# Kernel optimization log

Measured on AMD Instinct MI355X. Metric: run time of the kernel, lower is better.

## Reference

```python
import jax, jax.numpy as jnp
import numpy as np

P = 16        # patch size
IMG = 224     # image H=W
C = 3         # channels
D = 768       # projection_dim (= patch flatten dim here)
H = 12        # num heads
M = D // 4    # new_size = flattened_size / shrink_ratio(4) = 192
L = 6         # transformer layers
N = (IMG // P) ** 2   # 196 patches
FF = 3072     # dense_units[0]
HEAD = 512    # dense_units[2]
NCLS = 1000
EPS = 1e-6
B = 32


def setup_inputs() -> dict:
    key = jax.random.key(0)
    ks = iter(jax.random.split(key, 40))
    u = lambda shape, s=0.02: jax.random.uniform(next(ks), shape, jnp.float32, -s, s)
    image = jax.random.normal(next(ks), (B, IMG, IMG, C), jnp.float32)
    return dict(
        image=image,
        patch_w=u((P * P * C, D)), patch_b=u((D,)), pos_emb=u((N, D)),
        qw=u((L, D, M, H)), qb=jnp.zeros((L, M, H), jnp.float32),
        kw=u((L, D, M, H)), kb=jnp.zeros((L, M, H), jnp.float32),
        vw=u((L, D, M, H)), vb=jnp.zeros((L, M, H), jnp.float32),
        ow1=u((L, H * N, N)), ob1=jnp.zeros((L, M, N), jnp.float32),
        ow2=u((L, M, D)), ob2=jnp.zeros((L, N, D), jnp.float32),
        d1w=u((L, D, FF)), d1b=u((L, FF)),
        d2w=u((L, FF, D)), d2b=u((L, D)),
        head_w=u((N * D, HEAD), 0.005), head_b=u((HEAD,)),
        cls_w=u((HEAD, NCLS)), cls_b=u((NCLS,)),
    )


def _ln(x):
    # ViT_Custom_LayerNormalization: moments over axes [0,1,2] (all elements of [B,N,D])
    m = jnp.mean(x)
    v = jnp.mean(jnp.square(x - m))
    return (x - m) / jnp.sqrt(v + EPS)


def _gelu(x):
    return jax.nn.gelu(x, approximate=False)  # keras 'gelu' default is exact


def _forward(image, patch_w, patch_b, pos_emb, qw, qb, kw, kb, vw, vb,
             ow1, ob1, ow2, ob2, d1w, d1b, d2w, d2b, head_w, head_b, cls_w, cls_b):
    b = image.shape[0]
    # tf.image.extract_patches with VALID, stride=patch: [B,N,p*p*C] row-major patches
    patches = image.reshape(b, IMG // P, P, IMG // P, P, C)
    patches = patches.transpose(0, 1, 3, 2, 4, 5).reshape(b, N, P * P * C)
    x = patches @ patch_w + patch_b + pos_emb  # patch encode + pos embedding
    scale = 1.0 / np.float32(np.sqrt(D))       # key_dim = projection_dim
    for l in range(L):
        x1 = _ln(x)
        # per-head 3-D tensordot projections: [B,N,D] x [D,M,H] -> [B,N,M,H]
        q = jnp.einsum('bnd,dmh->bnmh', x1, qw[l]) + qb[l]
        k = jnp.einsum('bnd,dmh->bnmh', x1, kw[l]) + kb[l]
        v = jnp.einsum('bnd,dmh->bnmh', x1, vw[l]) + vb[l]
        att = jnp.einsum('bnmh,bNmh->bhnN', q, k) * scale  # [B,H,N,N]
        a = jax.nn.softmax(att, axis=-1)
        # attn @ V, then the module's transpose/unstack-concat -> [B,M,H*N] head-major
        o = jnp.einsum('bhnN,bNmh->bmhn', a, v).reshape(b, M, H * N)
        t = (o @ ow1[l] + ob1[l]).transpose(0, 2, 1)  # [B,N,M]
        attn_out = t @ ow2[l] + ob2[l]                # [B,N,D]
        x2 = attn_out + x
        x3 = _ln(x2)
        h = _gelu(x3 @ d1w[l] + d1b[l])
        h = _gelu(h @ d2w[l] + d2b[l])
        x = h + x2
    x = _ln(x)
    flat = x.reshape(b, N * D)
    feat = _gelu(flat @ head_w + head_b)
    return feat @ cls_w + cls_b  # [B, NCLS]


def reference(image, patch_w, patch_b, pos_emb, qw, qb, kw, kb, vw, vb,
              ow1, ob1, ow2, ob2, d1w, d1b, d2w, d2b, head_w, head_b, cls_w, cls_b):
    return _forward(image, patch_w, patch_b, pos_emb, qw, qb, kw, kb, vw, vb,
                    ow1, ob1, ow2, ob2, d1w, d1b, d2w, d2b, head_w, head_b, cls_w, cls_b)
```

## Files before the change

kernel.cpp:

```cpp
#include <hip/hip_runtime.h>
#include <cmath>

#define BZ    32
#define NP    196
#define DDIM  768
#define NHEAD 12
#define MDIM  192
#define NLAY  6
#define FFDIM 3072
#define HEADU 512
#define NCLS  1000
#define KHEAD 150528
#define BND   4816896
#define NPART 294

typedef __bf16 bf16_t;
typedef __bf16 bf16x8 __attribute__((ext_vector_type(8)));
typedef __bf16 bf16x4 __attribute__((ext_vector_type(4)));
typedef float  f32x4  __attribute__((ext_vector_type(4)));
typedef float  f32x2  __attribute__((ext_vector_type(2)));

#define OB_X      0L
#define OB_R      19267584L
#define OB_XB     38535168L
#define OB_XQKV   48168960L
#define OB_VT     134873088L
#define OB_O      165543936L
#define OB_T      194641920L
#define OB_WQKV   197050368L
#define OB_WO1    260751360L
#define OB_WO2    268025856L
#define OB_WD1    269795328L
#define OB_WD2    298106880L
#define OB_WPAT   326418432L
#define OB_BQKV   327598080L
#define OB_OB1T   327763968L
#define OB_RED    328667136L
#define OB_FEAT   328675584L

#define VT_SSTRIDE  39936L
#define ATTN_LDSP   93184
#define ATTN_LDS    143360
#define G256_LDS    98304
#define XROW        13824

__device__ __forceinline__ float gelu_exact(float x){
    return 0.5f * x * (1.0f + erff(x * 0.70710678118654752f));
}

__device__ __forceinline__ void gld16(const void* g, void* l){
    __builtin_amdgcn_global_load_lds((const __attribute__((address_space(1))) void*)g,
                                     (__attribute__((address_space(3))) void*)l, 16, 0, 0);
}

__global__ void __launch_bounds__(256)
patch_extract_k(const float* __restrict__ img, bf16_t* __restrict__ out)
{
    long idx = (long)blockIdx.x * 256 + threadIdx.x;
    if (idx >= (long)BND) return;
    int k = (int)(idx % DDIM);
    long bn = idx / DDIM;
    int n = (int)(bn % NP);
    int b = (int)(bn / NP);
    int c  = k % 3;
    int pj = (k / 3) % 16;
    int pi = k / 48;
    int gi = n / 14, gj = n % 14;
    long src = (((long)(b * 224 + gi * 16 + pi)) * 224 + (gj * 16 + pj)) * 3 + c;
    out[idx] = (bf16_t)img[src];
}

__global__ void __launch_bounds__(256)
wconv_k(const float* __restrict__ in, bf16_t* __restrict__ out,
        int IR, int IC, long OLD, int perm, int padTo, long inZ, long outZ)
{
    __shared__ float tile[32][33];
    int tid = threadIdx.x, tx = tid & 31, ty = tid >> 5;
    int c0 = blockIdx.x * 32, r0 = blockIdx.y * 32;
    const float* inz = in + (long)blockIdx.z * inZ;
    bf16_t* outz = out + (long)blockIdx.z * outZ;
    #pragma unroll
    for (int i = 0; i < 4; i++){
        int r = r0 + ty + 8*i, c = c0 + tx;
        tile[ty + 8*i][tx] = (r < IR && c < IC) ? inz[(long)r * IC + c] : 0.f;
    }
    __syncthreads();
    #pragma unroll
    for (int i = 0; i < 4; i++){
        int c = c0 + ty + 8*i, r = r0 + tx;
        if (c < IC && r < padTo){
            long pc = perm ? (long)(c % 12) * 192 + c / 12 : (long)c;
            outz[pc * OLD + r] = (bf16_t)tile[tx][ty + 8*i];
        }
    }
}

__global__ void __launch_bounds__(256)
gather_bias_k(const float* __restrict__ qb, const float* __restrict__ kb,
              const float* __restrict__ vb, float* __restrict__ out)
{
    int tid = blockIdx.x * 256 + threadIdx.x;
    int l = blockIdx.y;
    if (tid >= 6912) return;
    int g = tid / 2304, w = tid % 2304;
    int h = w / 192, m = w % 192;
    const float* src = (g == 0) ? qb : (g == 1) ? kb : vb;
    out[l*6912 + tid] = src[l*2304 + m * 12 + h];
}

__global__ void __launch_bounds__(256)
tr_bias_k(const float* __restrict__ ob1, float* __restrict__ out)
{
    int idx = blockIdx.x * 256 + threadIdx.x;
    int l = blockIdx.y;
    if (idx >= 37632) return;
    int n = idx / 192, m = idx - n*192;
    out[(long)l*37632 + idx] = ob1[(long)l*37632 + m*196 + n];
}

__global__ void __launch_bounds__(256)
zero_pad_o_k(bf16_t* __restrict__ o)
{
    int idx = blockIdx.x * 256 + threadIdx.x;
    if (idx >= 6144*16) return;
    int r = idx >> 4, j = idx & 15;
    o[(long)r * 2368 + 2352 + j] = (bf16_t)0.f;
}

__global__ void __launch_bounds__(256)
tr_v_k(const bf16_t* __restrict__ X, bf16_t* __restrict__ VT)
{
    __shared__ bf16_t tile[32][33];
    int tid = threadIdx.x, tx = tid & 31, ty = tid >> 5;
    int s = blockIdx.z, b = s & 31, h = s >> 5;
    int m0 = blockIdx.x * 32, n0 = blockIdx.y * 32;
    #pragma unroll
    for (int i = 0; i < 4; i++){
        int r = n0 + ty + 8*i, c = m0 + tx;
        tile[ty + 8*i][tx] = (r < 196) ?
            X[(long)(b*196 + r) * 6912 + 4608 + h*192 + c] : (bf16_t)0.f;
    }
    __syncthreads();
    #pragma unroll
    for (int i = 0; i < 4; i++){
        int m = m0 + ty + 8*i, n = n0 + tx;
        if (n < 208)
            VT[(long)s * VT_SSTRIDE + (long)m * 208 + n] = tile[tx][ty + 8*i];
    }
}

__global__ void __launch_bounds__(256)
ln_apply_k(const float* __restrict__ x, bf16_t* __restrict__ yb, float* __restrict__ yf,
           const float* __restrict__ psum, const float* __restrict__ psq, int npart)
{
    __shared__ float sred[8];
    int tid = threadIdx.x;
    float s = 0.f, q = 0.f;
    for (int i = tid; i < npart; i += 256){ s += psum[i]; q += psq[i]; }
    #pragma unroll
    for (int off = 32; off > 0; off >>= 1){ s += __shfl_xor(s, off); q += __shfl_xor(q, off); }
    if ((tid & 63) == 0){ sred[(tid>>6)*2] = s; sred[(tid>>6)*2+1] = q; }
    __syncthreads();
    s = sred[0] + sred[2] + sred[4] + sred[6];
    q = sred[1] + sred[3] + sred[5] + sred[7];
    float mean = s / (float)BND;
    float inv  = rsqrtf(q / (float)BND - mean*mean + 1e-6f);

    long i = (long)blockIdx.x * 256 + tid;
    if (i >= BND / 4) return;
    float4 v = ((const float4*)x)[i];
    v.x = (v.x - mean) * inv;
    v.y = (v.y - mean) * inv;
    v.z = (v.z - mean) * inv;
    v.w = (v.w - mean) * inv;
    bf16x4 o4 = { (bf16_t)v.x, (bf16_t)v.y, (bf16_t)v.z, (bf16_t)v.w };
    ((bf16x4*)yb)[i] = o4;
    if (yf) ((float4*)yf)[i] = v;
}

__global__ void __launch_bounds__(256)
attn_fused_k(const bf16_t* __restrict__ XQKV, const bf16_t* __restrict__ VT,
             bf16_t* __restrict__ O)
{
    extern __shared__ char lds[];
    const int tid = threadIdx.x, lane = tid & 63, w = tid >> 6;
    const int fr = lane & 15, kc = lane >> 4;
    const int s = blockIdx.y, qhalf = blockIdx.x;
    const int q0 = qhalf * 112;
    const int b = s & 31, h = s >> 5;
    const float scale = 0.03608439182435161f;
    const char* Xb = (const char*)XQKV + (long)(b*196) * XROW;
    const char* Qs = Xb + h*384;
    const char* Ks = Xb + 4608 + h*384;
    const char* Vs = (const char*)(VT + (long)s * VT_SSTRIDE);

    for (int t = 0; t < 23; t++){
        int idx = t*256 + tid;
        if (idx < 5824){
            int row = idx / 28, sl = idx - row*28;
            bool val = (sl < 24) && (row < 196);
            const char* src = Ks + (val ? ((long)row*XROW + ((sl*16) ^ ((row & 7) << 4))) : 0);
            gld16(src, lds + idx*16);
        }
    }
    asm volatile("s_waitcnt vmcnt(0)");
    __syncthreads();

    float pv_all[2][13][4];
    #pragma unroll
    for (int ii = 0; ii < 2; ii++){
        int i = w + ii*4;
        if (i >= 7) continue;
        f32x4 sa[13];
        #pragma unroll
        for (int f = 0; f < 13; f++) sa[f] = (f32x4){0.f,0.f,0.f,0.f};
        int qr = q0 + i*16 + fr; if (qr > 195) qr = 195;
        #pragma unroll
        for (int c = 0; c < 6; c++){
            bf16x8 av = *(const bf16x8*)(Qs + (long)qr*XROW + c*64 + kc*16);
            #pragma unroll
            for (int f = 0; f < 13; f++){
                int krow = f*16 + fr;
                bf16x8 bv = *(const bf16x8*)(lds + krow*448 + ((c*64 + kc*16) ^ ((krow & 7) << 4)));
                sa[f] = __builtin_amdgcn_mfma_f32_16x16x32_bf16(av, bv, sa[f], 0, 0, 0);
            }
        }
        #pragma unroll
        for (int r = 0; r < 4; r++){
            float mx = -1e30f;
            #pragma unroll
            for (int f = 0; f < 13; f++)
                if (f*16 + fr < 196) mx = fmaxf(mx, sa[f][r] * scale);
            mx = fmaxf(mx, __shfl_xor(mx, 1));
            mx = fmaxf(mx, __shfl_xor(mx, 2));
            mx = fmaxf(mx, __shfl_xor(mx, 4));
            mx = fmaxf(mx, __shfl_xor(mx, 8));
            float sum = 0.f;
            #pragma unroll
            for (int f = 0; f < 13; f++){
                float pv = (f*16 + fr < 196) ? __expf(sa[f][r] * scale - mx) : 0.f;
                pv_all[ii][f][r] = pv; sum += pv;
            }
            sum += __shfl_xor(sum, 1);
            sum += __shfl_xor(sum, 2);
            sum += __shfl_xor(sum, 4);
            sum += __shfl_xor(sum, 8);
            float inv = 1.f / sum;
            #pragma unroll
            for (int f = 0; f < 13; f++) pv_all[ii][f][r] *= inv;
        }
        #pragma unroll
        for (int f = 0; f < 13; f++)
            #pragma unroll
            for (int r = 0; r < 4; r++){
                int row = i*16 + kc*4 + r;
                int cb = (f*16 + fr) * 2;
                int a = ATTN_LDSP + row*448 + (cb < 384 ? (cb ^ ((row & 7) << 4)) : cb);
                *(bf16_t*)(lds + a) = (bf16_t)pv_all[ii][f][r];
            }
        if (lane < 32){
            int row = i*16 + (lane >> 1);
            *(f32x4*)(lds + ATTN_LDSP + row*448 + 416 + (lane & 1)*16) = (f32x4){0.f,0.f,0.f,0.f};
        }
    }
    __syncthreads();

    for (int t = 0; t < 21; t++){
        int idx = t*256 + tid;
        int row = idx / 28, sl = idx - row*28;
        bool val = (sl < 26);
        int cb = (sl < 24) ? ((sl*16) ^ ((row & 7) << 4)) : sl*16;
        const char* src = Vs + (val ? (row*416 + cb) : 0);
        gld16(src, lds + idx*16);
    }
    asm volatile("s_waitcnt vmcnt(0)");
    __syncthreads();

    f32x4 oa2[2][12];
    #pragma unroll
    for (int ii = 0; ii < 2; ii++){
        int i = w + ii*4;
        #pragma unroll
        for (int f = 0; f < 12; f++) oa2[ii][f] = (f32x4){0.f,0.f,0.f,0.f};
        if (i >= 7) continue;
        #pragma unroll
        for (int c = 0; c < 7; c++){
            int prow = i*16 + fr;
            int cb = c*64 + kc*16;
            int acb = (cb < 384) ? (cb ^ ((prow & 7) << 4)) : cb;
            bf16x8 av = *(const bf16x8*)(lds + ATTN_LDSP + prow*448 + acb);
            #pragma unroll
            for (int f = 0; f < 12; f++){
                int vrow = f*16 + fr;
                int bcb = (cb < 384) ? (cb ^ ((vrow & 7) << 4)) : cb;
                bf16x8 bv = *(const bf16x8*)(lds + vrow*448 + bcb);
                oa2[ii][f] = __builtin_amdgcn_mfma_f32_16x16x32_bf16(av, bv, oa2[ii][f], 0, 0, 0);
            }
        }
    }
    __syncthreads();

    #pragma unroll
    for (int ii = 0; ii < 2; ii++){
        int i = w + ii*4;
        if (i >= 7) continue;
        #pragma unroll
        for (int f = 0; f < 12; f++){
            int m = f*16 + fr;
            #pragma unroll
            for (int r = 0; r < 4; r++){
                int nl = i*16 + kc*4 + r;
                *(bf16_t*)(lds + m*232 + nl*2) = (bf16_t)oa2[ii][f][r];
            }
        }
    }
    __syncthreads();
    const int nch = (qhalf == 0) ? 28 : 21;
    const int total = 192 * nch;
    char* ob = (char*)O + ((long)(b*192))*4736 + ((long)(h*196 + q0))*2;
    for (int idx = tid; idx < total; idx += 256){
        int m = idx / nch, ch = idx - m*nch;
        f32x2 v2 = *(const f32x2*)(lds + m*232 + ch*8);
        *(f32x2*)(ob + (long)m*4736 + ch*8) = v2;
    }
}

__global__ void __launch_bounds__(512, 2)
gemm256_k(const bf16_t* __restrict__ A, long ldA,
          const bf16_t* __restrict__ B, long ldB,
          bf16_t* __restrict__ C, long ldC,
          const float* __restrict__ bias1,
          int Md, int Nd, int Kd, int G, int doGelu)
{
    extern __shared__ char gsm[];
    const int tid = threadIdx.x;
    const int lane = tid & 63, w = tid >> 6;
    const int wm = w >> 2, wn = w & 3;

    int gx = gridDim.x, gy = gridDim.y;
    int n2d = gx * gy;
    int flat = blockIdx.x + gx * blockIdx.y;
    int q8 = n2d >> 3, r8 = n2d & 7;
    int xcd = flat & 7, pos = flat >> 3;
    int lid = (xcd < r8 ? xcd*(q8+1) : r8*(q8+1) + (xcd-r8)*q8) + pos;
    int fullg = gx / G;
    int fullsz = fullg * G * gy;
    int bx, by;
    if (lid < fullsz){
        int gsz = G * gy;
        int g = lid / gsz, rem = lid - g*gsz;
        by = rem / G; bx = g*G + (rem - by*G);
    } else {
        int tw = gx - fullg*G;
        int rem = lid - fullsz;
        by = rem / tw; bx = fullg*G + (rem - by*tw);
    }
    const int row0 = by * 256, col0 = bx * 256;

    f32x4 acc[8][4];
    #pragma unroll
    for (int i = 0; i < 8; i++)
        #pragma unroll
        for (int j = 0; j < 4; j++)
            acc[i][j] = (f32x4){0.f, 0.f, 0.f, 0.f};

    const int fr = lane & 15, kc = lane >> 4;
    const int swz = (fr >> 1) & 3;
    int aOff[8], bOff[4];
    #pragma unroll
    for (int i = 0; i < 8; i++)
        aOff[i] = (wm*128 + i*16 + fr) * 64 + ((kc ^ swz) << 4);
    #pragma unroll
    for (int j = 0; j < 4; j++)
        bOff[j] = (wn*64 + j*16 + fr) * 64 + ((kc ^ swz) << 4);

    auto stage = [&](int buf, int kt){
        long kOff = (long)kt * 32;
        char* base = gsm + buf * 32768;
        #pragma unroll
        for (int r = 0; r < 2; r++){
            int idx = r*512 + tid;
            int row = idx >> 2, cp = idx & 3;
            int cc = cp ^ ((row >> 1) & 3);
            int ar = row0 + row; if (ar >= Md) ar = Md - 1;
            int br = col0 + row; if (br >= Nd) br = Nd - 1;
            gld16((const void*)(A + (long)ar*ldA + kOff + cc*8), (void*)(base + row*64 + cp*16));
            gld16((const void*)(B + (long)br*ldB + kOff + cc*8), (void*)(base + 16384 + row*64 + cp*16));
        }
    };

    const int nt = Kd >> 5;
    stage(0, 0);
    stage(1, 1);
    asm volatile("s_waitcnt vmcnt(4)" ::: "memory");
    __builtin_amdgcn_s_barrier();
    __builtin_amdgcn_sched_barrier(0);

    for (int t = 0; t < nt; t++){
        int cur = t % 3;
        if (t + 2 < nt) stage((t + 2) % 3, t + 2);
        const char* baseA = gsm + cur * 32768;
        const char* baseB = baseA + 16384;
        bf16x8 av[8], bv[4];
        #pragma unroll
        for (int i = 0; i < 8; i++) av[i] = *(const bf16x8*)(baseA + aOff[i]);
        #pragma unroll
        for (int j = 0; j < 4; j++) bv[j] = *(const bf16x8*)(baseB + bOff[j]);
        __builtin_amdgcn_s_setprio(1);
        #pragma unroll
        for (int i = 0; i < 8; i++)
            #pragma unroll
            for (int j = 0; j < 4; j++)
                acc[i][j] = __builtin_amdgcn_mfma_f32_16x16x32_bf16(av[i], bv[j], acc[i][j], 0, 0, 0);
        __builtin_amdgcn_s_setprio(0);
        if (t + 2 < nt)      asm volatile("s_waitcnt vmcnt(4)" ::: "memory");
        else if (t + 1 < nt) asm volatile("s_waitcnt vmcnt(0)" ::: "memory");
        __builtin_amdgcn_s_barrier();
        __builtin_amdgcn_sched_barrier(0);
    }

    #pragma unroll
    for (int i = 0; i < 8; i++){
        int gmb = row0 + wm*128 + i*16 + kc*4;
        #pragma unroll
        for (int j = 0; j < 4; j++){
            int gn = col0 + wn*64 + j*16 + fr;
            if (gn >= Nd) continue;
            float b1 = bias1 ? bias1[gn] : 0.f;
            #pragma unroll
            for (int r = 0; r < 4; r++){
                int gm = gmb + r;
                if (gm >= Md) continue;
                float v = acc[i][j][r] + b1;
                if (doGelu) v = gelu_exact(v);
                C[(long)gm*ldC + gn] = (bf16_t)v;
            }
        }
    }
}

__global__ void __launch_bounds__(256)
mfma_gemm_k(const bf16_t* __restrict__ A, long ldA, long sA,
            const bf16_t* __restrict__ B, long ldB, long sB,
            void* __restrict__ C, long ldC, long sC,
            const float* __restrict__ Cadd,
            const float* __restrict__ bias1,
            const float* __restrict__ bias2, int b2mod, int b2ld,
            int Md, int Nd, int Kd, float alpha, int doGelu, int mode,
            float* __restrict__ psum, float* __restrict__ psq, int redN, int G)
{
    __shared__ bf16_t sm[3][2][128][32];
    __shared__ float redbuf[8];
    const int tid = threadIdx.x;
    const int lane = tid & 63, w = tid >> 6;
    const int wm = w >> 1, wn = w & 1;
    const int z = blockIdx.z;

    int n2d = gridDim.x * gridDim.y;
    int flat = blockIdx.x + gridDim.x * blockIdx.y;
    int q8 = n2d >> 3, r8 = n2d & 7;
    int xcd = flat & 7, pos = flat >> 3;
    int lid = (xcd < r8 ? xcd*(q8+1) : r8*(q8+1) + (xcd-r8)*q8) + pos;
    int gx = gridDim.x, gy = gridDim.y;
    int fullg = gx / G;
    int fullsz = fullg * G * gy;
    int bx, by;
    if (lid < fullsz){
        int gsz = G * gy;
        int g = lid / gsz, rem = lid - g*gsz;
        by = rem / G; bx = g*G + (rem - by*G);
    } else {
        int tw = gx - fullg*G;
        int rem = lid - fullsz;
        by = rem / tw; bx = fullg*G + (rem - by*tw);
    }

    const int row0 = by * 128, col0 = bx * 128;

    const bf16_t* Ab = A + (long)z * sA + (long)row0 * ldA;
    const bf16_t* Bb = B + (long)z * sB + (long)col0 * ldB;

    f32x4 acc[4][4];
    #pragma unroll
    for (int i = 0; i < 4; i++)
        #pragma unroll
        for (int j = 0; j < 4; j++)
            acc[i][j] = (f32x4){0.f, 0.f, 0.f, 0.f};

    const int fr = lane & 15, kc = lane >> 4;
    const int swz = (fr >> 1) & 3;
    int aOff[4], bOff[4];
    #pragma unroll
    for (int i = 0; i < 4; i++){
        aOff[i] = (wm*64 + i*16 + fr) * 64 + ((kc ^ swz) << 4);
        bOff[i] = (wn*64 + i*16 + fr) * 64 + ((kc ^ swz) << 4);
    }

    auto stage = [&](int buf, int kt){
        long kOff = (long)kt * 32;
        #pragma unroll
        for (int r = 0; r < 2; r++){
            int idx = r*256 + tid;
            int row = idx >> 2, cp = idx & 3;
            int cc = cp ^ ((row >> 1) & 3);
            gld16((const void*)(Ab + (long)row*ldA + kOff + cc*8), (void*)&sm[buf][0][row][cp*8]);
            gld16((const void*)(Bb + (long)row*ldB + kOff + cc*8), (void*)&sm[buf][1][row][cp*8]);
        }
    };

    const int nt = Kd >> 5;
    stage(0, 0);
    stage(1, 1);
    asm volatile("s_waitcnt vmcnt(4)" ::: "memory");
    __builtin_amdgcn_s_barrier();
    __builtin_amdgcn_sched_barrier(0);

    for (int t = 0; t < nt; t++){
        int cur = t % 3;
        if (t + 2 < nt) stage((t + 2) % 3, t + 2);
        const char* baseA = (const char*)sm + cur * 16384;
        const char* baseB = baseA + 8192;
        bf16x8 av[4], bv[4];
        #pragma unroll
        for (int i = 0; i < 4; i++){
            av[i] = *(const bf16x8*)(baseA + aOff[i]);
            bv[i] = *(const bf16x8*)(baseB + bOff[i]);
        }
        __builtin_amdgcn_s_setprio(1);
        #pragma unroll
        for (int i = 0; i < 4; i++)
            #pragma unroll
            for (int j = 0; j < 4; j++)
                acc[i][j] = __builtin_amdgcn_mfma_f32_16x16x32_bf16(av[i], bv[j], acc[i][j], 0, 0, 0);
        __builtin_amdgcn_s_setprio(0);
        if (t + 2 < nt)      asm volatile("s_waitcnt vmcnt(4)" ::: "memory");
        else if (t + 1 < nt) asm volatile("s_waitcnt vmcnt(0)" ::: "memory");
        __builtin_amdgcn_s_barrier();
        __builtin_amdgcn_sched_barrier(0);
    }

    float rs = 0.f, rq = 0.f;
    #pragma unroll
    for (int i = 0; i < 4; i++){
        int gmb = row0 + wm*64 + i*16 + kc*4;
        #pragma unroll
        for (int j = 0; j < 4; j++){
            int gn = col0 + wn*64 + j*16 + fr;
            if (gn >= Nd) continue;
            #pragma unroll
            for (int r = 0; r < 4; r++){
                int gm = gmb + r;
                if (gm >= Md) continue;
                float v = alpha * acc[i][j][r];
                if (bias1) v += bias1[gn];
                if (bias2) v += bias2[(long)(gm % b2mod) * b2ld + gn];
                if (doGelu) v = gelu_exact(v);
                if (mode == 0){
                    long off = (long)z*sC + (long)gm*ldC + gn;
                    if (Cadd) v += Cadd[off];
                    ((float*)C)[off] = v;
                    rs += v; rq += v*v;
                } else {
                    ((bf16_t*)C)[(long)z*sC + (long)gm*ldC + gn] = (bf16_t)v;
                }
            }
        }
    }

    if (redN > 0){
        #pragma unroll
        for (int off = 32; off > 0; off >>= 1){
            rs += __shfl_xor(rs, off); rq += __shfl_xor(rq, off);
        }
        if (lane == 0){ redbuf[w] = rs; redbuf[4 + w] = rq; }
        __syncthreads();
        if (tid == 0){
            psum[flat] = redbuf[0] + redbuf[1] + redbuf[2] + redbuf[3];
            psq[flat]  = redbuf[4] + redbuf[5] + redbuf[6] + redbuf[7];
        }
    }
}

__global__ void __launch_bounds__(256)
gemm64_k(const bf16_t* __restrict__ A, long ldA, long sA,
         const bf16_t* __restrict__ B, long ldB, long sB,
         bf16_t* __restrict__ C, long ldC, long sC,
         const float* __restrict__ bias2, int b2ld,
         int Md, int Nd, int Kd)
{
    __shared__ bf16_t sm[3][2][64][32];
    const int tid = threadIdx.x;
    const int lane = tid & 63, w = tid >> 6;
    const int wm = w >> 1, wn = w & 1;
    const int z = blockIdx.z;
    const int row0 = blockIdx.y * 64, col0 = blockIdx.x * 64;

    const bf16_t* Ab = A + (long)z * sA + (long)row0 * ldA;
    const bf16_t* Bb = B + (long)z * sB + (long)col0 * ldB;

    f32x4 acc[2][2];
    #pragma unroll
    for (int i = 0; i < 2; i++)
        #pragma unroll
        for (int j = 0; j < 2; j++)
            acc[i][j] = (f32x4){0.f,0.f,0.f,0.f};

    const int fr = lane & 15, kc = lane >> 4;
    const int swz = (fr >> 1) & 3;
    int aOff[2], bOff[2];
    #pragma unroll
    for (int i = 0; i < 2; i++){
        aOff[i] = (wm*32 + i*16 + fr) * 64 + ((kc ^ swz) << 4);
        bOff[i] = (wn*32 + i*16 + fr) * 64 + ((kc ^ swz) << 4);
    }

    auto stage = [&](int buf, int kt){
        long kOff = (long)kt * 32;
        int row = tid >> 2, cp = tid & 3;
        int cc = cp ^ ((row >> 1) & 3);
        gld16((const void*)(Ab + (long)row*ldA + kOff + cc*8), (void*)&sm[buf][0][row][cp*8]);
        gld16((const void*)(Bb + (long)row*ldB + kOff + cc*8), (void*)&sm[buf][1][row][cp*8]);
    };

    const int nt = Kd >> 5;
    stage(0, 0);
    stage(1, 1);
    asm volatile("s_waitcnt vmcnt(2)" ::: "memory");
    __builtin_amdgcn_s_barrier();
    __builtin_amdgcn_sched_barrier(0);

    for (int t = 0; t < nt; t++){
        int cur = t % 3;
        if (t + 2 < nt) stage((t + 2) % 3, t + 2);
        const char* baseA = (const char*)sm + cur * 8192;
        const char* baseB = baseA + 4096;
        bf16x8 av[2], bv[2];
        #pragma unroll
        for (int i = 0; i < 2; i++){
            av[i] = *(const bf16x8*)(baseA + aOff[i]);
            bv[i] = *(const bf16x8*)(baseB + bOff[i]);
        }
        __builtin_amdgcn_s_setprio(1);
        #pragma unroll
        for (int i = 0; i < 2; i++)
            #pragma unroll
            for (int j = 0; j < 2; j++)
                acc[i][j] = __builtin_amdgcn_mfma_f32_16x16x32_bf16(av[i], bv[j], acc[i][j], 0, 0, 0);
        __builtin_amdgcn_s_setprio(0);
        if (t + 2 < nt)      asm volatile("s_waitcnt vmcnt(2)" ::: "memory");
        else if (t + 1 < nt) asm volatile("s_waitcnt vmcnt(0)" ::: "memory");
        __builtin_amdgcn_s_barrier();
        __builtin_amdgcn_sched_barrier(0);
    }

    #pragma unroll
    for (int i = 0; i < 2; i++){
        int gmb = row0 + wm*32 + i*16 + kc*4;
        #pragma unroll
        for (int j = 0; j < 2; j++){
            int gn = col0 + wn*32 + j*16 + fr;
            if (gn >= Nd) continue;
            #pragma unroll
            for (int r = 0; r < 4; r++){
                int gm = gmb + r;
                if (gm >= Md) continue;
                float v = acc[i][j][r];
                if (bias2) v += bias2[(long)gm * b2ld + gn];
                C[(long)z*sC + (long)gm*ldC + gn] = (bf16_t)v;
            }
        }
    }
}

__global__ void __launch_bounds__(256)
head_splitk_k(const float* __restrict__ A, const float* __restrict__ W, float* __restrict__ feat)
{
    __shared__ float As[16][36];
    __shared__ float Bs[16][68];
    int col0 = blockIdx.x * 64;
    long kbase = (long)blockIdx.y * 2352;
    int tid = threadIdx.x, tx = tid & 15, ty = tid >> 4;
    float acc[2][4] = {};
    for (int k0 = 0; k0 < 2352; k0 += 16){
        #pragma unroll
        for (int u = 0; u < 2; u++){
            int idx = tid * 2 + u;
            int m = idx >> 4, kk = idx & 15;
            As[kk][m] = A[(long)m * KHEAD + kbase + k0 + kk];
        }
        #pragma unroll
        for (int u = 0; u < 4; u++){
            int idx = tid * 4 + u;
            int kk = idx >> 6, n = idx & 63;
            Bs[kk][n] = W[(kbase + k0 + kk) * 512 + col0 + n];
        }
        __syncthreads();
        #pragma unroll
        for (int kk = 0; kk < 16; kk++){
            float a0 = As[kk][ty*2], a1 = As[kk][ty*2+1];
            float b0 = Bs[kk][tx*4], b1 = Bs[kk][tx*4+1], b2 = Bs[kk][tx*4+2], b3 = Bs[kk][tx*4+3];
            acc[0][0] += a0*b0; acc[0][1] += a0*b1; acc[0][2] += a0*b2; acc[0][3] += a0*b3;
            acc[1][0] += a1*b0; acc[1][1] += a1*b1; acc[1][2] += a1*b2; acc[1][3] += a1*b3;
        }
        __syncthreads();
    }
    #pragma unroll
    for (int i = 0; i < 2; i++)
        #pragma unroll
        for (int j = 0; j < 4; j++)
            atomicAdd(&feat[(ty*2 + i) * 512 + col0 + tx*4 + j], acc[i][j]);
}

__global__ void __launch_bounds__(256)
cls_k(const float* __restrict__ feat, const float* __restrict__ hb,
      const float* __restrict__ W, const float* __restrict__ bias, float* __restrict__ out)
{
    __shared__ float fs[512];
    int b = blockIdx.y;
    int j = blockIdx.x * 256 + threadIdx.x;
    for (int i = threadIdx.x; i < 512; i += 256)
        fs[i] = gelu_exact(feat[b * 512 + i] + hb[i]);
    __syncthreads();
    if (j < NCLS){
        float s = bias[j];
        for (int k = 0; k < 512; k++) s += fs[k] * W[(long)k * NCLS + j];
        out[b * NCLS + j] = s;
    }
}

extern "C" void kernel_launch(void* const* d_in, const int* in_sizes, int n_in,
                              void* d_out, int out_size, void* d_ws, size_t ws_size,
                              hipStream_t stream)
{
    const float* image   = (const float*)d_in[0];
    const float* patch_w = (const float*)d_in[1];
    const float* patch_b = (const float*)d_in[2];
    const float* pos_emb = (const float*)d_in[3];
    const float* qw  = (const float*)d_in[4];
    const float* qb  = (const float*)d_in[5];
    const float* kw  = (const float*)d_in[6];
    const float* kb  = (const float*)d_in[7];
    const float* vw  = (const float*)d_in[8];
    const float* vb  = (const float*)d_in[9];
    const float* ow1 = (const float*)d_in[10];
    const float* ob1 = (const float*)d_in[11];
    const float* ow2 = (const float*)d_in[12];
    const float* ob2 = (const float*)d_in[13];
    const float* d1w = (const float*)d_in[14];
    const float* d1b = (const float*)d_in[15];
    const float* d2w = (const float*)d_in[16];
    const float* d2b = (const float*)d_in[17];
    const float* head_w = (const float*)d_in[18];
    const float* head_b = (const float*)d_in[19];
    const float* cls_w  = (const float*)d_in[20];
    const float* cls_b  = (const float*)d_in[21];

    char* wsb = (char*)d_ws;
    float*  X    = (float*) (wsb + OB_X);
    float*  R    = (float*) (wsb + OB_R);
    bf16_t* XB   = (bf16_t*)(wsb + OB_XB);
    bf16_t* XQKV = (bf16_t*)(wsb + OB_XQKV);
    bf16_t* VT   = (bf16_t*)(wsb + OB_VT);
    bf16_t* O    = (bf16_t*)(wsb + OB_O);
    bf16_t* Tt   = (bf16_t*)(wsb + OB_T);
    bf16_t* H1   = XQKV;
    bf16_t* PATB = XQKV;
    bf16_t* WQKV = (bf16_t*)(wsb + OB_WQKV);
    bf16_t* WO1  = (bf16_t*)(wsb + OB_WO1);
    bf16_t* WO2  = (bf16_t*)(wsb + OB_WO2);
    bf16_t* WD1  = (bf16_t*)(wsb + OB_WD1);
    bf16_t* WD2  = (bf16_t*)(wsb + OB_WD2);
    bf16_t* WPAT = (bf16_t*)(wsb + OB_WPAT);
    float*  BQKV = (float*) (wsb + OB_BQKV);
    float*  OB1T = (float*) (wsb + OB_OB1T);
    float*  PS   = (float*) (wsb + OB_RED);
    float*  PQ   = PS + 512;
    float*  FEAT = (float*) (wsb + OB_FEAT);
    float*  out  = (float*)d_out;

    hipFuncSetAttribute((const void*)attn_fused_k,
                        hipFuncAttributeMaxDynamicSharedMemorySize, ATTN_LDS);
    hipFuncSetAttribute((const void*)gemm256_k,
                        hipFuncAttributeMaxDynamicSharedMemorySize, G256_LDS);

    auto pickG = [](int Kd){
        int g = (3*1024*1024) / (128 * Kd * 2);
        if (g > 8) g = 8;
        if (g < 1) g = 1;
        return g;
    };
    auto mg = [&](const bf16_t* A, long ldA, long sA, const bf16_t* B, long ldB, long sB,
                  void* C, long ldC, long sC, const float* Cadd, const float* b1,
                  const float* b2, int b2mod, int b2ld,
                  int Md, int Nd, int Kd, int nb, float alpha, int gelu, int mode, int redN){
        dim3 g((Nd + 127) / 128, (Md + 127) / 128, nb);
        mfma_gemm_k<<<g, 256, 0, stream>>>(A, ldA, sA, B, ldB, sB, C, ldC, sC,
                                           Cadd, b1, b2, b2mod, b2ld,
                                           Md, Nd, Kd, alpha, gelu, mode, PS, PQ, redN,
                                           pickG(Kd));
    };
    auto wconv = [&](const float* in, bf16_t* o_, int IR, int IC, int perm, long OLD,
                     int padTo, int nz, long inZ, long outZ){
        dim3 g((IC + 31) / 32, (padTo + 31) / 32, nz);
        wconv_k<<<g, 256, 0, stream>>>(in, o_, IR, IC, OLD, perm, padTo, inZ, outZ);
    };
    auto lnapply = [&](const float* in, bf16_t* ob, float* of){
        ln_apply_k<<<4704, 256, 0, stream>>>(in, ob, of, PS, PQ, NPART);
    };

    wconv(patch_w, WPAT, 768, 768, 0, 768, 768, 1, 0, 0);
    wconv(qw, WQKV,               768, 2304, 1, 768, 768, 6, 768L*2304, 6912L*768);
    wconv(kw, WQKV + 2304L*768,   768, 2304, 1, 768, 768, 6, 768L*2304, 6912L*768);
    wconv(vw, WQKV + 4608L*768,   768, 2304, 1, 768, 768, 6, 768L*2304, 6912L*768);
    wconv(ow1, WO1, 2352, 196, 0, 2368, 2368, 6, 2352L*196, 606208L);
    wconv(ow2, WO2, 192, 768, 0, 192, 192, 6, 147456L, 147456L);
    wconv(d1w, WD1, 768, 3072, 0, 768, 768, 6, 2359296L, 2359296L);
    wconv(d2w, WD2, 3072, 768, 0, 3072, 3072, 6, 2359296L, 2359296L);
    gather_bias_k<<<dim3(27, 6), 256, 0, stream>>>(qb, kb, vb, BQKV);
    tr_bias_k<<<dim3(147, 6), 256, 0, stream>>>(ob1, OB1T);

    patch_extract_k<<<18816, 256, 0, stream>>>(image, PATB);
    mg(PATB, 768, 0, WPAT, 768, 0, X, 768, 0,
       nullptr, patch_b, pos_emb, 196, 768, 6272, 768, 768, 1, 1.f, 0, 0, NPART);
    zero_pad_o_k<<<384, 256, 0, stream>>>(O);

    for (int l = 0; l < NLAY; l++){
        lnapply(X, XB, nullptr);
        gemm256_k<<<dim3(27, 25), 512, G256_LDS, stream>>>(
            XB, 768, WQKV + (long)l*6912*768, 768, XQKV, 6912,
            BQKV + l*6912, 6272, 6912, 768, 4, 0);
        tr_v_k<<<dim3(6, 7, 384), 256, 0, stream>>>(XQKV, VT);
        attn_fused_k<<<dim3(2, 384), 256, ATTN_LDS, stream>>>(XQKV, VT, O);
        gemm64_k<<<dim3(3, 4, 32), 256, 0, stream>>>(
            WO1 + (long)l*606208, 2368, 0, O, 2368, 192L*2368, Tt, 192, 37632,
            OB1T + (long)l*37632, 192, 196, 192, 2368);
        mg(Tt, 192, 0, WO2 + (long)l*147456, 192, 0, R, 768, 0, X, nullptr,
           ob2 + (long)l*196*768, 196, 768, 6272, 768, 192, 1, 1.f, 0, 0, NPART);
        lnapply(R, XB, nullptr);
        gemm256_k<<<dim3(12, 25), 512, G256_LDS, stream>>>(
            XB, 768, WD1 + (long)l*2359296, 768, H1, 3072,
            d1b + l*3072, 6272, 3072, 768, 4, 1);
        mg(H1, 3072, 0, WD2 + (long)l*2359296, 3072, 0, X, 768, 0, R,
           d2b + l*768, nullptr, 1, 1, 6272, 768, 3072, 1, 1.f, 1, 0, NPART);
    }

    lnapply(X, XB, R);
    hipMemsetAsync(FEAT, 0, BZ * HEADU * sizeof(float), stream);
    head_splitk_k<<<dim3(8, 64), 256, 0, stream>>>(R, head_w, FEAT);
    cls_k<<<dim3(4, 32), 256, 0, stream>>>(FEAT, head_b, cls_w, cls_b, out);
    (void)in_sizes; (void)n_in; (void)out_size; (void)ws_size;
}
```

Measured before the change: 3.444 ms.

## Split-K the FFN down-projection and fuse bias, GELU, residual and LN stats

The second FFN GEMM (K=3072, only 6x49 tiles) now runs as a 2-way split-K, each half writing fp32 partials to a new workspace slice. A new elementwise kernel sums the partials, adds bias, applies GELU and the residual, and produces per-block LayerNorm partial sums, so ln_apply reads 4704 partials instead of 294. The first FFN GEMM moves from gemm256_k to the 128-tile mfma_gemm_k, and the QKV GEMM's grouping parameter goes from 4 to 8. The aim is more parallelism on the under-filled GEMM, at the cost of extra fp32 partial traffic and one more launch per layer.

```diff
diff --git a/kernel.cpp b/kernel.cpp
--- a/kernel.cpp
+++ b/kernel.cpp
@@ -13,6 +13,7 @@
 #define KHEAD 150528
 #define BND   4816896
 #define NPART 294
+#define NPARTF 4704
 
 typedef __bf16 bf16_t;
 typedef __bf16 bf16x8 __attribute__((ext_vector_type(8)));
@@ -24,6 +25,7 @@
 #define OB_R      19267584L
 #define OB_XB     38535168L
 #define OB_XQKV   48168960L
+#define OB_P0     86704128L
 #define OB_VT     134873088L
 #define OB_O      165543936L
 #define OB_T      194641920L
@@ -36,7 +38,7 @@
 #define OB_BQKV   327598080L
 #define OB_OB1T   327763968L
 #define OB_RED    328667136L
-#define OB_FEAT   328675584L
+#define OB_FEAT   328704768L
 
 #define VT_SSTRIDE  39936L
 #define ATTN_LDSP   93184
@@ -176,6 +178,36 @@
     bf16x4 o4 = { (bf16_t)v.x, (bf16_t)v.y, (bf16_t)v.z, (bf16_t)v.w };
     ((bf16x4*)yb)[i] = o4;
     if (yf) ((float4*)yf)[i] = v;
+}
+
+__global__ void __launch_bounds__(256)
+ffn2_finish_k(const float* __restrict__ P, const float* __restrict__ R,
+              const float* __restrict__ d2b, float* __restrict__ X,
+              float* __restrict__ psum, float* __restrict__ psq)
+{
+    __shared__ float redbuf[8];
+    int tid = threadIdx.x;
+    long i = (long)blockIdx.x * 256 + tid;
+    float4 a = ((const float4*)P)[i];
+    float4 b = ((const float4*)(P + 4816896))[i];
+    float4 r = ((const float4*)R)[i];
+    int col = (int)((i * 4) % 768);
+    float v0 = gelu_exact(a.x + b.x + d2b[col])     + r.x;
+    float v1 = gelu_exact(a.y + b.y + d2b[col + 1]) + r.y;
+    float v2 = gelu_exact(a.z + b.z + d2b[col + 2]) + r.z;
+    float v3 = gelu_exact(a.w + b.w + d2b[col + 3]) + r.w;
+    float4 o; o.x = v0; o.y = v1; o.z = v2; o.w = v3;
+    ((float4*)X)[i] = o;
+    float rs = v0 + v1 + v2 + v3;
+    float rq = v0*v0 + v1*v1 + v2*v2 + v3*v3;
+    #pragma unroll
+    for (int off = 32; off > 0; off >>= 1){ rs += __shfl_xor(rs, off); rq += __shfl_xor(rq, off); }
+    if ((tid & 63) == 0){ redbuf[(tid>>6)*2] = rs; redbuf[(tid>>6)*2+1] = rq; }
+    __syncthreads();
+    if (tid == 0){
+        psum[blockIdx.x] = redbuf[0] + redbuf[2] + redbuf[4] + redbuf[6];
+        psq[blockIdx.x]  = redbuf[1] + redbuf[3] + redbuf[5] + redbuf[7];
+    }
 }
 
 __global__ void __launch_bounds__(256)
@@ -456,6 +488,9 @@
     const int wm = w >> 1, wn = w & 1;
     const int z = blockIdx.z;
 
+    long kStart = 0; int KdL = Kd; long zA = z;
+    if (mode == 7){ kStart = (long)z * (Kd >> 1); KdL = Kd >> 1; zA = 0; }
+
     int n2d = gridDim.x * gridDim.y;
     int flat = blockIdx.x + gridDim.x * blockIdx.y;
     int q8 = n2d >> 3, r8 = n2d & 7;
@@ -477,8 +512,8 @@
 
     const int row0 = by * 128, col0 = bx * 128;
 
-    const bf16_t* Ab = A + (long)z * sA + (long)row0 * ldA;
-    const bf16_t* Bb = B + (long)z * sB + (long)col0 * ldB;
+    const bf16_t* Ab = A + zA * sA + (long)row0 * ldA + kStart;
+    const bf16_t* Bb = B + zA * sB + (long)col0 * ldB + kStart;
 
     f32x4 acc[4][4];
     #pragma unroll
@@ -508,7 +543,7 @@
         }
     };
 
-    const int nt = Kd >> 5;
+    const int nt = KdL >> 5;
     stage(0, 0);
     stage(1, 1);
     asm volatile("s_waitcnt vmcnt(4)" ::: "memory");
@@ -560,6 +595,8 @@
                     if (Cadd) v += Cadd[off];
                     ((float*)C)[off] = v;
                     rs += v; rq += v*v;
+                } else if (mode == 7){
+                    ((float*)C)[(long)z*sC + (long)gm*ldC + gn] = v;
                 } else {
                     ((bf16_t*)C)[(long)z*sC + (long)gm*ldC + gn] = (bf16_t)v;
                 }
@@ -760,6 +797,7 @@
     float*  R    = (float*) (wsb + OB_R);
     bf16_t* XB   = (bf16_t*)(wsb + OB_XB);
     bf16_t* XQKV = (bf16_t*)(wsb + OB_XQKV);
+    float*  P0   = (float*) (wsb + OB_P0);
     bf16_t* VT   = (bf16_t*)(wsb + OB_VT);
     bf16_t* O    = (bf16_t*)(wsb + OB_O);
     bf16_t* Tt   = (bf16_t*)(wsb + OB_T);
@@ -774,7 +812,7 @@
     float*  BQKV = (float*) (wsb + OB_BQKV);
     float*  OB1T = (float*) (wsb + OB_OB1T);
     float*  PS   = (float*) (wsb + OB_RED);
-    float*  PQ   = PS + 512;
+    float*  PQ   = PS + NPARTF;
     float*  FEAT = (float*) (wsb + OB_FEAT);
     float*  out  = (float*)d_out;
 
@@ -804,8 +842,8 @@
         dim3 g((IC + 31) / 32, (padTo + 31) / 32, nz);
         wconv_k<<<g, 256, 0, stream>>>(in, o_, IR, IC, OLD, perm, padTo, inZ, outZ);
     };
-    auto lnapply = [&](const float* in, bf16_t* ob, float* of){
-        ln_apply_k<<<4704, 256, 0, stream>>>(in, ob, of, PS, PQ, NPART);
+    auto lnapply = [&](const float* in, bf16_t* ob, float* of, int npart){
+        ln_apply_k<<<4704, 256, 0, stream>>>(in, ob, of, PS, PQ, npart);
     };
 
     wconv(patch_w, WPAT, 768, 768, 0, 768, 768, 1, 0, 0);
@@ -825,10 +863,10 @@
     zero_pad_o_k<<<384, 256, 0, stream>>>(O);
 
     for (int l = 0; l < NLAY; l++){
-        lnapply(X, XB, nullptr);
+        lnapply(X, XB, nullptr, l == 0 ? NPART : NPARTF);
         gemm256_k<<<dim3(27, 25), 512, G256_LDS, stream>>>(
             XB, 768, WQKV + (long)l*6912*768, 768, XQKV, 6912,
-            BQKV + l*6912, 6272, 6912, 768, 4, 0);
+            BQKV + l*6912, 6272, 6912, 768, 8, 0);
         tr_v_k<<<dim3(6, 7, 384), 256, 0, stream>>>(XQKV, VT);
         attn_fused_k<<<dim3(2, 384), 256, ATTN_LDS, stream>>>(XQKV, VT, O);
         gemm64_k<<<dim3(3, 4, 32), 256, 0, stream>>>(
@@ -836,15 +874,15 @@
             OB1T + (long)l*37632, 192, 196, 192, 2368);
         mg(Tt, 192, 0, WO2 + (long)l*147456, 192, 0, R, 768, 0, X, nullptr,
            ob2 + (long)l*196*768, 196, 768, 6272, 768, 192, 1, 1.f, 0, 0, NPART);
-        lnapply(R, XB, nullptr);
-        gemm256_k<<<dim3(12, 25), 512, G256_LDS, stream>>>(
-            XB, 768, WD1 + (long)l*2359296, 768, H1, 3072,
-            d1b + l*3072, 6272, 3072, 768, 4, 1);
-        mg(H1, 3072, 0, WD2 + (long)l*2359296, 3072, 0, X, 768, 0, R,
-           d2b + l*768, nullptr, 1, 1, 6272, 768, 3072, 1, 1.f, 1, 0, NPART);
-    }
-
-    lnapply(X, XB, R);
+        lnapply(R, XB, nullptr, NPART);
+        mg(XB, 768, 0, WD1 + (long)l*2359296, 768, 0, H1, 3072, 0, nullptr,
+           d1b + l*3072, nullptr, 1, 1, 6272, 3072, 768, 1, 1.f, 1, 1, 0);
+        mg(H1, 3072, 0, WD2 + (long)l*2359296, 3072, 0, P0, 768, 4816896, nullptr,
+           nullptr, nullptr, 1, 1, 6272, 768, 3072, 2, 1.f, 0, 7, 0);
+        ffn2_finish_k<<<4704, 256, 0, stream>>>(P0, R, d2b + l*768, X, PS, PQ);
+    }
+
+    lnapply(X, XB, R, NPARTF);
     hipMemsetAsync(FEAT, 0, BZ * HEADU * sizeof(float), stream);
     head_splitk_k<<<dim3(8, 64), 256, 0, stream>>>(R, head_w, FEAT);
     cls_k<<<dim3(4, 32), 256, 0, stream>>>(FEAT, head_b, cls_w, cls_b, out);
```

Result: faster. 3.177 ms (-7.8%).
